# Kernel tuning notes

Measured on AMD Instinct MI355X. Metric: run time of the kernel, lower is better.

Reference implementation:

```python
import jax, jax.numpy as jnp
import numpy as np

CODE_SIZE = 1024
CODE_DIM = 256
B, H, W = 64, 32, 32

def setup_inputs() -> dict:
    key = jax.random.key(0)
    k1, k2 = jax.random.split(key)
    x = jax.random.normal(k1, (B, CODE_DIM, H, W), dtype=jnp.float32)
    # nn.Embedding weight initialized uniform(-1/code_size, 1/code_size)
    weight = jax.random.uniform(k2, (CODE_SIZE, CODE_DIM), dtype=jnp.float32,
                                minval=-1.0 / CODE_SIZE, maxval=1.0 / CODE_SIZE)
    return {"x": x, "weight": weight}

def reference(x, weight):
    b, c, h, w = x.shape
    # (B,C,H,W) -> (B*H*W, C)
    flat = jnp.transpose(x, (0, 2, 3, 1)).reshape(-1, c)
    # squared euclidean distances; argmin of d^2 equals argmin of cdist(p=2)
    d2 = (jnp.sum(flat * flat, axis=1, keepdims=True)
          - 2.0 * (flat @ weight.T)
          + jnp.sum(weight * weight, axis=1)[None, :])  # (N, code_size)
    idxs = jnp.argmin(d2, axis=1).reshape(b, h, w)       # (B,H,W) int
    quantized = jnp.transpose(weight[idxs], (0, 3, 1, 2))  # (B,C,H,W)
    ste = jax.lax.stop_gradient(quantized - x) + x        # straight-through
    return quantized, ste, idxs
```

## Files before the change

kernel.cpp:

```cpp
#include <hip/hip_runtime.h>
#include <math.h>

typedef float vf4 __attribute__((ext_vector_type(4)));

#define CODE_SIZE 1024
#define CODE_DIM  256
#define BB        64
#define HWSZ      1024
#define NROWS     (BB * HWSZ)
#define QELEMS    (BB * CODE_DIM * HWSZ)

__global__ void k_sumsq_w(const float* __restrict__ w, float* __restrict__ sw) {
#pragma clang fp contract(off)
  const int code = blockIdx.x * blockDim.x + threadIdx.x;
  if (code >= CODE_SIZE) return;
  const float* row = w + (size_t)code * CODE_DIM;
  float halves[2];
  for (int h = 0; h < 2; ++h) {
    const float* p = row + h * 128;
    float r[8];
#pragma unroll
    for (int j = 0; j < 8; ++j) { float v = p[j]; r[j] = v * v; }
    for (int i = 8; i < 128; i += 8) {
#pragma unroll
      for (int j = 0; j < 8; ++j) { float v = p[i + j]; r[j] += v * v; }
    }
    halves[h] = ((r[0] + r[1]) + (r[2] + r[3])) + ((r[4] + r[5]) + (r[6] + r[7]));
  }
  sw[code] = halves[0] + halves[1];
}

__global__ void k_sumsq_x(const float* __restrict__ x, float* __restrict__ sx) {
#pragma clang fp contract(off)
  const int n = blockIdx.x * blockDim.x + threadIdx.x;
  const int b = n >> 10, hw = n & 1023;
  const float* p = x + (size_t)b * CODE_DIM * HWSZ + hw;
  float halves[2];
  for (int h = 0; h < 2; ++h) {
    const float* q = p + (size_t)(h * 128) * HWSZ;
    float r[8];
#pragma unroll
    for (int j = 0; j < 8; ++j) { float v = q[(size_t)j * HWSZ]; r[j] = v * v; }
    for (int i = 8; i < 128; i += 8) {
#pragma unroll
      for (int j = 0; j < 8; ++j) { float v = q[(size_t)(i + j) * HWSZ]; r[j] += v * v; }
    }
    halves[h] = ((r[0] + r[1]) + (r[2] + r[3])) + ((r[4] + r[5]) + (r[6] + r[7]));
  }
  sx[n] = halves[0] + halves[1];
}

#define MT  64
#define NTC 256
#define NCH (CODE_SIZE / NTC)
#define KC  32

__launch_bounds__(256, 4)
__global__ void k_argmin(const float* __restrict__ x, const float* __restrict__ w,
                         const float* __restrict__ sx, const float* __restrict__ sw,
                         float* __restrict__ oidx) {
  __shared__ float xs[KC * MT];
  __shared__ float ws[KC * NTC];

  const int t   = threadIdx.x;
  const int n0  = blockIdx.x * MT;
  const int b   = n0 >> 10;
  const int hw0 = n0 & 1023;
  const int rt  = t & 7;
  const int ct  = t >> 3;

  float bk[8]; float bi[8];
#pragma unroll
  for (int ri = 0; ri < 8; ++ri) { bk[ri] = INFINITY; bi[ri] = (float)CODE_SIZE; }

  for (int chunk = 0; chunk < NCH; ++chunk) {
    const int code0 = chunk * NTC;

    float acc[8][8];
#pragma unroll
    for (int ri = 0; ri < 8; ++ri)
#pragma unroll
      for (int cj = 0; cj < 8; ++cj) acc[ri][cj] = 0.0f;

    for (int kc = 0; kc < CODE_DIM / KC; ++kc) {
      const int kbase = kc * KC;
      __syncthreads();
      {
#pragma unroll
        for (int i = 0; i < 2; ++i) {
          const int j  = t + 256 * i;
          const int k  = j >> 4;
          const int rq = j & 15;
          vf4 v = *(const vf4*)(x + ((size_t)(b * CODE_DIM + kbase + k) * HWSZ + hw0 + rq * 4));
          *(vf4*)(xs + k * MT + rq * 4) = v;
        }
      }
      {
        const float* wr = w + (size_t)(code0 + t) * CODE_DIM + kbase;
#pragma unroll
        for (int q = 0; q < 8; ++q) {
          vf4 v = *(const vf4*)(wr + q * 4);
          ws[(q * 4 + 0) * NTC + t] = v.x;
          ws[(q * 4 + 1) * NTC + t] = v.y;
          ws[(q * 4 + 2) * NTC + t] = v.z;
          ws[(q * 4 + 3) * NTC + t] = v.w;
        }
      }
      __syncthreads();

      const float* xp = xs + rt * 8;
      const float* wp = ws + ct * 8;
#pragma unroll 4
      for (int k = 0; k < KC; ++k) {
        vf4 xv0 = *(const vf4*)(xp + k * MT);
        vf4 xv1 = *(const vf4*)(xp + k * MT + 4);
        vf4 wv0 = *(const vf4*)(wp + k * NTC);
        vf4 wv1 = *(const vf4*)(wp + k * NTC + 4);
        float xr[8] = {xv0.x, xv0.y, xv0.z, xv0.w, xv1.x, xv1.y, xv1.z, xv1.w};
        float wc[8] = {wv0.x, wv0.y, wv0.z, wv0.w, wv1.x, wv1.y, wv1.z, wv1.w};
#pragma unroll
        for (int ri = 0; ri < 8; ++ri)
#pragma unroll
          for (int cj = 0; cj < 8; ++cj)
            acc[ri][cj] = fmaf(xr[ri], wc[cj], acc[ri][cj]);
      }
    }

    {
#pragma clang fp contract(off)
      float sxr[8];
#pragma unroll
      for (int ri = 0; ri < 8; ++ri) sxr[ri] = sx[n0 + rt * 8 + ri];
#pragma unroll
      for (int cj = 0; cj < 8; ++cj) {
        const int code = code0 + ct * 8 + cj;
        const float swv = sw[code];
        const float codef = (float)code;
#pragma unroll
        for (int ri = 0; ri < 8; ++ri) {
          const float tmp = sxr[ri] - 2.0f * acc[ri][cj];
          const float key = tmp + swv;
          if (key < bk[ri] || (key == bk[ri] && codef < bi[ri])) {
            bk[ri] = key; bi[ri] = codef;
          }
        }
      }
    }
  }

  __syncthreads();
  float* redk = ws;
  float* redi = ws + 32 * MT;
#pragma unroll
  for (int ri = 0; ri < 8; ++ri) {
    const int row = rt * 8 + ri;
    redk[ct * MT + row] = bk[ri];
    redi[ct * MT + row] = bi[ri];
  }
  __syncthreads();
  if (t < MT) {
    float k0 = redk[t]; float i0 = redi[t];
    for (int q = 1; q < 32; ++q) {
      const float kq = redk[q * MT + t];
      const float iq = redi[q * MT + t];
      if (kq < k0 || (kq == k0 && iq < i0)) { k0 = kq; i0 = iq; }
    }
    oidx[n0 + t] = i0;
  }
}

#define WT_S 65

__global__ void k_epilogue(const float* __restrict__ x, const float* __restrict__ w,
                           const float* __restrict__ oidx, float* __restrict__ out) {
#pragma clang fp contract(off)
  __shared__ int   idxs[MT];
  __shared__ float wt[CODE_DIM * WT_S];

  const int t   = threadIdx.x;
  const int n0  = blockIdx.x * MT;
  const int b   = n0 >> 10;
  const int hw0 = n0 & 1023;

  if (t < MT) idxs[t] = (int)oidx[n0 + t];
  __syncthreads();

#pragma unroll
  for (int i = 0; i < 16; ++i) {
    const int j  = t + 256 * i;
    const int r  = j & 63;
    const int cq = j >> 6;
    vf4 v = *(const vf4*)(w + (size_t)idxs[r] * CODE_DIM + cq * 4);
    wt[(cq * 4 + 0) * WT_S + r] = v.x;
    wt[(cq * 4 + 1) * WT_S + r] = v.y;
    wt[(cq * 4 + 2) * WT_S + r] = v.z;
    wt[(cq * 4 + 3) * WT_S + r] = v.w;
  }
  __syncthreads();

#pragma unroll
  for (int i = 0; i < 16; ++i) {
    const int j  = t + 256 * i;
    const int c  = j >> 4;
    const int rq = j & 15;
    const size_t off = (size_t)(b * CODE_DIM + c) * HWSZ + hw0 + rq * 4;
    vf4 xv = *(const vf4*)(x + off);
    vf4 q, s;
#pragma unroll
    for (int u = 0; u < 4; ++u) {
      const float qv = wt[c * WT_S + rq * 4 + u];
      q[u] = qv;
      const float d = qv - xv[u];
      s[u] = d + xv[u];
    }
    *(vf4*)(out + off) = q;
    *(vf4*)(out + (size_t)QELEMS + off) = s;
  }
}

extern "C" void kernel_launch(void* const* d_in, const int* in_sizes, int n_in,
                              void* d_out, int out_size, void* d_ws, size_t ws_size,
                              hipStream_t stream) {
  const float* x = (const float*)d_in[0];
  const float* w = (const float*)d_in[1];
  float* out  = (float*)d_out;
  float* oidx = out + 2 * (size_t)QELEMS;
  float* sx = out + (size_t)QELEMS;
  float* sw = out + (size_t)QELEMS + NROWS;

  k_sumsq_w<<<CODE_SIZE / 256, 256, 0, stream>>>(w, sw);
  k_sumsq_x<<<NROWS / 256, 256, 0, stream>>>(x, sx);
  k_argmin<<<NROWS / MT, 256, 0, stream>>>(x, w, sx, sw, oidx);
  k_epilogue<<<NROWS / MT, 256, 0, stream>>>(x, w, oidx, out);
}
```

Before: 615.1 us.

## Restructure argmin to one code per thread with pre-transposed codebook

```diff
diff --git a/kernel.cpp b/kernel.cpp
--- a/kernel.cpp
+++ b/kernel.cpp
@@ -50,125 +50,128 @@
   sx[n] = halves[0] + halves[1];
 }
 
-#define MT  64
-#define NTC 256
-#define NCH (CODE_SIZE / NTC)
-#define KC  32
+__global__ void k_transpose(const float* __restrict__ w, float* __restrict__ wT) {
+  const int k = blockIdx.x;
+  const int t = threadIdx.x;
+#pragma unroll
+  for (int i = 0; i < 4; ++i) {
+    const int c = i * 256 + t;
+    wT[(size_t)k * CODE_SIZE + c] = w[(size_t)c * CODE_DIM + k];
+  }
+}
+
+#define RT 32
+#define KC 32
+#define NCHUNK 4
 
 __launch_bounds__(256, 4)
-__global__ void k_argmin(const float* __restrict__ x, const float* __restrict__ w,
+__global__ void k_argmin(const float* __restrict__ x, const float* __restrict__ wT,
                          const float* __restrict__ sx, const float* __restrict__ sw,
                          float* __restrict__ oidx) {
-  __shared__ float xs[KC * MT];
-  __shared__ float ws[KC * NTC];
+  __shared__ float ws[KC * 256];
+  __shared__ float r2k[256], r2i[256];
 
   const int t   = threadIdx.x;
-  const int n0  = blockIdx.x * MT;
+  const int n0  = blockIdx.x * RT;
   const int b   = n0 >> 10;
   const int hw0 = n0 & 1023;
-  const int rt  = t & 7;
-  const int ct  = t >> 3;
-
-  float bk[8]; float bi[8];
-#pragma unroll
-  for (int ri = 0; ri < 8; ++ri) { bk[ri] = INFINITY; bi[ri] = (float)CODE_SIZE; }
-
-  for (int chunk = 0; chunk < NCH; ++chunk) {
-    const int code0 = chunk * NTC;
-
-    float acc[8][8];
-#pragma unroll
-    for (int ri = 0; ri < 8; ++ri)
-#pragma unroll
-      for (int cj = 0; cj < 8; ++cj) acc[ri][cj] = 0.0f;
+
+  float rbk = INFINITY, rbi = (float)CODE_SIZE;
+
+  for (int chunk = 0; chunk < NCHUNK; ++chunk) {
+    const int code0 = chunk * 256;
+
+    float acc[RT];
+#pragma unroll
+    for (int r = 0; r < RT; ++r) acc[r] = 0.0f;
 
     for (int kc = 0; kc < CODE_DIM / KC; ++kc) {
-      const int kbase = kc * KC;
-      __syncthreads();
-      {
-#pragma unroll
-        for (int i = 0; i < 2; ++i) {
-          const int j  = t + 256 * i;
-          const int k  = j >> 4;
-          const int rq = j & 15;
-          vf4 v = *(const vf4*)(x + ((size_t)(b * CODE_DIM + kbase + k) * HWSZ + hw0 + rq * 4));
-          *(vf4*)(xs + k * MT + rq * 4) = v;
-        }
-      }
-      {
-        const float* wr = w + (size_t)(code0 + t) * CODE_DIM + kbase;
-#pragma unroll
-        for (int q = 0; q < 8; ++q) {
-          vf4 v = *(const vf4*)(wr + q * 4);
-          ws[(q * 4 + 0) * NTC + t] = v.x;
-          ws[(q * 4 + 1) * NTC + t] = v.y;
-          ws[(q * 4 + 2) * NTC + t] = v.z;
-          ws[(q * 4 + 3) * NTC + t] = v.w;
-        }
-      }
-      __syncthreads();
-
-      const float* xp = xs + rt * 8;
-      const float* wp = ws + ct * 8;
+      const int kb = kc * KC;
+      __syncthreads();
+#pragma unroll
+      for (int i = 0; i < 8; ++i) {
+        const int j  = t + 256 * i;
+        const int kk = j >> 6;
+        const int c4 = j & 63;
+        vf4 v = *(const vf4*)(wT + (size_t)(kb + kk) * CODE_SIZE + code0 + c4 * 4);
+        *(vf4*)(ws + kk * 256 + c4 * 4) = v;
+      }
+      __syncthreads();
+
+      const float* xbase = x + (size_t)(b * CODE_DIM + kb) * HWSZ + hw0;
 #pragma unroll 4
       for (int k = 0; k < KC; ++k) {
-        vf4 xv0 = *(const vf4*)(xp + k * MT);
-        vf4 xv1 = *(const vf4*)(xp + k * MT + 4);
-        vf4 wv0 = *(const vf4*)(wp + k * NTC);
-        vf4 wv1 = *(const vf4*)(wp + k * NTC + 4);
-        float xr[8] = {xv0.x, xv0.y, xv0.z, xv0.w, xv1.x, xv1.y, xv1.z, xv1.w};
-        float wc[8] = {wv0.x, wv0.y, wv0.z, wv0.w, wv1.x, wv1.y, wv1.z, wv1.w};
-#pragma unroll
-        for (int ri = 0; ri < 8; ++ri)
-#pragma unroll
-          for (int cj = 0; cj < 8; ++cj)
-            acc[ri][cj] = fmaf(xr[ri], wc[cj], acc[ri][cj]);
-      }
-    }
-
+        const float wv = ws[k * 256 + t];
+        const float* xr = xbase + (size_t)k * HWSZ;
+#pragma unroll
+        for (int r = 0; r < RT; ++r)
+          acc[r] = fmaf(xr[r], wv, acc[r]);
+      }
+    }
+
+    float key[RT];
     {
 #pragma clang fp contract(off)
-      float sxr[8];
-#pragma unroll
-      for (int ri = 0; ri < 8; ++ri) sxr[ri] = sx[n0 + rt * 8 + ri];
-#pragma unroll
-      for (int cj = 0; cj < 8; ++cj) {
-        const int code = code0 + ct * 8 + cj;
-        const float swv = sw[code];
-        const float codef = (float)code;
-#pragma unroll
-        for (int ri = 0; ri < 8; ++ri) {
-          const float tmp = sxr[ri] - 2.0f * acc[ri][cj];
-          const float key = tmp + swv;
-          if (key < bk[ri] || (key == bk[ri] && codef < bi[ri])) {
-            bk[ri] = key; bi[ri] = codef;
-          }
+      const int code = code0 + t;
+      const float swv = sw[code];
+#pragma unroll
+      for (int r = 0; r < RT; ++r) {
+        const float tmp = sx[n0 + r] - 2.0f * acc[r];
+        key[r] = tmp + swv;
+      }
+    }
+    const float codef = (float)(code0 + t);
+#pragma unroll
+    for (int h = 0; h < 2; ++h) {
+      float* redk = ws;
+      float* redi = ws + 16 * 256;
+      __syncthreads();
+#pragma unroll
+      for (int j = 0; j < 16; ++j) {
+        redk[j * 256 + t] = key[h * 16 + j];
+        redi[j * 256 + t] = codef;
+      }
+      __syncthreads();
+      {
+        const int row = t >> 4, seg = t & 15;
+        float k0 = INFINITY, i0 = (float)CODE_SIZE;
+        for (int c = 0; c < 16; ++c) {
+          const float kq = redk[row * 256 + seg * 16 + c];
+          const float iq = redi[row * 256 + seg * 16 + c];
+          if (kq < k0 || (kq == k0 && iq < i0)) { k0 = kq; i0 = iq; }
         }
-      }
-    }
-  }
-
-  __syncthreads();
-  float* redk = ws;
-  float* redi = ws + 32 * MT;
-#pragma unroll
-  for (int ri = 0; ri < 8; ++ri) {
-    const int row = rt * 8 + ri;
-    redk[ct * MT + row] = bk[ri];
-    redi[ct * MT + row] = bi[ri];
-  }
-  __syncthreads();
-  if (t < MT) {
-    float k0 = redk[t]; float i0 = redi[t];
-    for (int q = 1; q < 32; ++q) {
-      const float kq = redk[q * MT + t];
-      const float iq = redi[q * MT + t];
-      if (kq < k0 || (kq == k0 && iq < i0)) { k0 = kq; i0 = iq; }
-    }
-    oidx[n0 + t] = i0;
-  }
-}
-
+        r2k[t] = k0; r2i[t] = i0;
+      }
+      __syncthreads();
+      if ((t >> 4) == h && (t & 15) < 16) {
+      }
+      if (t < 16) {
+        const int row = h * 16 + t;
+        float k0 = r2k[t * 16], i0 = r2i[t * 16];
+        for (int s = 1; s < 16; ++s) {
+          const float kq = r2k[t * 16 + s];
+          const float iq = r2i[t * 16 + s];
+          if (kq < k0 || (kq == k0 && iq < i0)) { k0 = kq; i0 = iq; }
+        }
+        r2k[t] = k0; r2i[t] = i0;
+      }
+      __syncthreads();
+      if (t < RT) {
+        const int hh = t >> 4;
+        if (hh == h) {
+          const float kq = r2k[t & 15], iq = r2i[t & 15];
+          if (kq < rbk || (kq == rbk && iq < rbi)) { rbk = kq; rbi = iq; }
+        }
+      }
+      __syncthreads();
+    }
+  }
+
+  if (t < RT) oidx[n0 + t] = rbi;
+
+}
+
+#define MT 64
 #define WT_S 65
 
 __global__ void k_epilogue(const float* __restrict__ x, const float* __restrict__ w,
@@ -227,9 +230,11 @@
   float* oidx = out + 2 * (size_t)QELEMS;
   float* sx = out + (size_t)QELEMS;
   float* sw = out + (size_t)QELEMS + NROWS;
-
+  float* wT = out + (size_t)QELEMS + 131072;
+
+  k_transpose<<<CODE_DIM, 256, 0, stream>>>(w, wT);
   k_sumsq_w<<<CODE_SIZE / 256, 256, 0, stream>>>(w, sw);
   k_sumsq_x<<<NROWS / 256, 256, 0, stream>>>(x, sx);
-  k_argmin<<<NROWS / MT, 256, 0, stream>>>(x, w, sx, sw, oidx);
+  k_argmin<<<NROWS / RT, 256, 0, stream>>>(x, wT, sx, sw, oidx);
   k_epilogue<<<NROWS / MT, 256, 0, stream>>>(x, w, oidx, out);
 }
```

Measured after the change: 1.372 ms. 123% more time.
